# Kernel optimization log

Hardware: AMD Instinct MI355X
Metric: run time of the kernel (lower is better)

Reference implementation:

```python
import jax, jax.numpy as jnp
import numpy as np

B, T, U = 4, 256, 64
D_ENC, D_DEC, V = 512, 512, 1024
IN_F = D_ENC + D_DEC  # 1024


def setup_inputs() -> dict:
    key = jax.random.key(0)
    ks = jax.random.split(key, 10)
    enc = jax.random.normal(ks[0], (B, T, D_ENC), dtype=jnp.float32)
    dec = jax.random.normal(ks[1], (B, U, D_DEC), dtype=jnp.float32)
    # ragged lengths in [len/2, len]; force max to be attained so padded
    # shape equals the torch packed output shape (MaxPad == (T, U)).
    enc_lens = jax.random.randint(ks[2], (B,), T // 2, T + 1, dtype=jnp.int32).at[0].set(T)
    dec_lens = jax.random.randint(ks[3], (B,), U // 2, U + 1, dtype=jnp.int32).at[0].set(U)
    s_e = 1.0 / np.sqrt(D_ENC)
    s_d = 1.0 / np.sqrt(D_DEC)
    s_f = 1.0 / np.sqrt(IN_F)
    W_enc = jax.random.uniform(ks[4], (D_ENC, IN_F), jnp.float32, -s_e, s_e)
    b_enc = jax.random.uniform(ks[5], (IN_F,), jnp.float32, -s_e, s_e)
    W_dec = jax.random.uniform(ks[6], (D_DEC, IN_F), jnp.float32, -s_d, s_d)
    b_dec = jax.random.uniform(ks[7], (IN_F,), jnp.float32, -s_d, s_d)
    W_fc = jax.random.uniform(ks[8], (IN_F, V), jnp.float32, -s_f, s_f)
    b_fc = jax.random.uniform(ks[9], (V,), jnp.float32, -s_f, s_f)
    return dict(enc=enc, dec=dec, W_enc=W_enc, b_enc=b_enc, W_dec=W_dec,
                b_dec=b_dec, W_fc=W_fc, b_fc=b_fc,
                enc_lens=enc_lens, dec_lens=dec_lens)


def reference(enc, dec, W_enc, b_enc, W_dec, b_dec, W_fc, b_fc, enc_lens, dec_lens):
    # per-frame / per-label projections: [B,T,IN_F], [B,U,IN_F]
    pe = jnp.einsum('btd,df->btf', enc, W_enc) + b_enc
    pd = jnp.einsum('bud,df->buf', dec, W_dec) + b_dec
    # broadcast-add joint grid: [B,T,U,IN_F]
    h = pe[:, :, None, :] + pd[:, None, :, :]
    logits = jnp.einsum('btuf,fv->btuv', jnp.tanh(h), W_fc) + b_fc
    logp = jax.nn.log_softmax(logits, axis=-1)
    # zero out cells beyond (enc_len_b, dec_len_b), matching F.pad(value=0.)
    t_ok = jnp.arange(T)[None, :] < enc_lens[:, None]          # [B,T]
    u_ok = jnp.arange(U)[None, :] < dec_lens[:, None]          # [B,U]
    mask = (t_ok[:, :, None] & u_ok[:, None, :])[..., None]    # [B,T,U,1]
    return jnp.where(mask, logp, 0.0)
```

## Files before the change

### kernel.cpp

```cpp
#include <hip/hip_runtime.h>
#include <hip/hip_bf16.h>


#define TT 256
#define UU 64
#define VV 1024
#define FF 1024
#define DK 512

typedef __bf16 bf16x8 __attribute__((ext_vector_type(8)));
typedef float  f32x16 __attribute__((ext_vector_type(16)));
typedef int    i32x4v __attribute__((ext_vector_type(4)));
typedef int    i32x16 __attribute__((ext_vector_type(16)));

__device__ __forceinline__ float fast_tanh(float x) {
  float ax = __builtin_fabsf(x);
  float e  = __expf(-2.0f * ax);
  float r  = (1.0f - e) * __builtin_amdgcn_rcpf(1.0f + e);
  return __builtin_copysignf(r, x);
}

__global__ __launch_bounds__(256)
void prep_w(const float* __restrict__ Wenc, const float* __restrict__ Wdec,
            const float* __restrict__ Wfc,
            __bf16* __restrict__ Pen, __bf16* __restrict__ Pde,
            signed char* __restrict__ Pq, float* __restrict__ sc)
{
  int bi = blockIdx.x;
  int tid = threadIdx.x;
  if (bi < 512) {
    const float* W = (bi < 256) ? Wenc : Wdec;
    __bf16* P = (bi < 256) ? Pen : Pde;
    int base = (bi < 256) ? bi : bi - 256;
    int idx = base * 256 + tid;
    int k8 = idx >> 10, v = idx & 1023;
    bf16x8 o;
#pragma unroll
    for (int j = 0; j < 8; ++j) o[j] = (__bf16)W[(k8 * 8 + j) * 1024 + v];
    *(bf16x8*)(P + (size_t)idx * 8) = o;
    return;
  }
  __shared__ float mx[4][64];
  __shared__ float smax[64];
  int blk = bi - 512;
  int p = tid >> 6;
  int c = tid & 63;
  int v = blk * 64 + c;
  float m = 0.f;
#pragma unroll 8
  for (int k = p * 256; k < p * 256 + 256; ++k)
    m = fmaxf(m, __builtin_fabsf(Wfc[k * 1024 + v]));
  mx[p][c] = m;
  __syncthreads();
  float mm = fmaxf(fmaxf(mx[0][c], mx[1][c]), fmaxf(mx[2][c], mx[3][c]));
  if (p == 0) { smax[c] = mm; sc[v] = (mm > 0.f) ? mm / 127.f : 1.f; }
  __syncthreads();
  float si = (smax[c] > 0.f) ? 127.f / smax[c] : 0.f;
  for (int k16 = p * 16; k16 < p * 16 + 16; ++k16) {
    unsigned int w[4];
#pragma unroll
    for (int g = 0; g < 4; ++g) {
      unsigned int a = 0;
#pragma unroll
      for (int j = 0; j < 4; ++j) {
        float x = Wfc[(k16 * 16 + g * 4 + j) * 1024 + v];
        int q = (int)rintf(x * si);
        q = q > 127 ? 127 : (q < -127 ? -127 : q);
        a |= (unsigned int)(q & 255) << (8 * j);
      }
      w[g] = a;
    }
    *(uint4*)(Pq + ((size_t)k16 * 1024 + v) * 16) = make_uint4(w[0], w[1], w[2], w[3]);
  }
}

__global__ __launch_bounds__(256)
void proj_mfma(const float* __restrict__ enc, const float* __restrict__ dec,
               const __bf16* __restrict__ Pen, const __bf16* __restrict__ Pde,
               const float* __restrict__ be, const float* __restrict__ bd,
               float* __restrict__ pe, float* __restrict__ pd)
{
  constexpr int BK = 128;
  __shared__ __align__(16) char As[2][64 * BK * 2];
  const int tid = threadIdx.x;
  const int lane = tid & 63;
  const int wid  = tid >> 6;
  const int l31  = lane & 31;
  const int lhi  = lane >> 5;

  int bi = blockIdx.x;
  const float* X; const __bf16* PW; const float* bias; float* P; int rt, ct;
  if (bi < 64) { X = enc; PW = Pen; bias = be; P = pe; rt = bi >> 2; ct = bi & 3; }
  else { int bj = bi - 64; X = dec; PW = Pde; bias = bd; P = pd; rt = bj >> 2; ct = bj & 3; }
  const int r0 = rt * 64;

  auto fillA = [&](int buf, int kc) {
#pragma unroll
    for (int i = 0; i < 4; ++i) {
      int tau = i * 256 + tid;
      int r = tau >> 4, g = tau & 15;
      int k = kc * BK + g * 8;
      const float4* x4 = (const float4*)(X + (r0 + r) * DK + k);
      float4 a0 = x4[0], a1 = x4[1];
      float xv[8] = {a0.x, a0.y, a0.z, a0.w, a1.x, a1.y, a1.z, a1.w};
      bf16x8 p;
#pragma unroll
      for (int q = 0; q < 8; ++q) p[q] = (__bf16)xv[q];
      *(bf16x8*)(&As[buf][r * (BK * 2) + ((g * 16) ^ ((r & 7) << 4))]) = p;
    }
  };

  f32x16 acc[2][2];
#pragma unroll
  for (int mi = 0; mi < 2; ++mi)
#pragma unroll
    for (int ni = 0; ni < 2; ++ni)
#pragma unroll
      for (int q = 0; q < 16; ++q) acc[mi][ni][q] = 0.f;

  fillA(0, 0);
  __syncthreads();
  const int colBase = ct * 256 + wid * 64 + l31;
  for (int kc = 0; kc < DK / BK; ++kc) {
    if (kc + 1 < DK / BK) fillA((kc + 1) & 1, kc + 1);
    const char* Ab = As[kc & 1];
#pragma unroll 2
    for (int ks = 0; ks < BK / 16; ++ks) {
      int k8 = (kc * 8 + ks) * 2 + lhi;
      bf16x8 bfr[2];
#pragma unroll
      for (int ni = 0; ni < 2; ++ni)
        bfr[ni] = *(const bf16x8*)(PW + ((size_t)k8 * VV + colBase + ni * 32) * 8);
      bf16x8 afr[2];
#pragma unroll
      for (int mi = 0; mi < 2; ++mi) {
        int ra = mi * 32 + l31;
        int kb = ks * 32 + lhi * 16;
        afr[mi] = *(const bf16x8*)(&Ab[ra * (BK * 2) + (kb ^ ((ra & 7) << 4))]);
      }
#pragma unroll
      for (int mi = 0; mi < 2; ++mi)
#pragma unroll
        for (int ni = 0; ni < 2; ++ni)
          acc[mi][ni] = __builtin_amdgcn_mfma_f32_32x32x16_bf16(afr[mi], bfr[ni], acc[mi][ni], 0, 0, 0);
    }
    __syncthreads();
  }
  float bv[2];
#pragma unroll
  for (int ni = 0; ni < 2; ++ni) bv[ni] = bias[colBase + ni * 32];
#pragma unroll
  for (int mi = 0; mi < 2; ++mi)
#pragma unroll
    for (int j = 0; j < 16; ++j) {
      int row = r0 + mi * 32 + (j & 3) + 8 * (j >> 2) + 4 * lhi;
#pragma unroll
      for (int ni = 0; ni < 2; ++ni)
        P[row * VV + colBase + ni * 32] = acc[mi][ni][j] + bv[ni];
    }
}

__global__ __launch_bounds__(512, 2)
void joint_main(const float* __restrict__ pe, const float* __restrict__ pd,
                const signed char* __restrict__ Pq, const float* __restrict__ sc,
                const float* __restrict__ bfc,
                const int* __restrict__ elens, const int* __restrict__ dlens,
                float* __restrict__ out)
{
  __shared__ __align__(16) unsigned char Bb[4][32768];
  __shared__ __align__(16) unsigned char Ab[2][4096];
  __shared__ float pr[8][64];
  __shared__ float lseS[64];

  const int blk = blockIdx.x;
  const int b = blk >> 8;
  const int t = blk & 255;
  const int tid = threadIdx.x;
  const int elen = elens[b], dlen = dlens[b];
  float* outBase = out + (size_t)blk * (UU * VV);

  if (t >= elen) {
    float4 z = {0.f, 0.f, 0.f, 0.f};
#pragma unroll 4
    for (int i = tid; i < UU * VV / 4; i += 512) ((float4*)outBase)[i] = z;
    return;
  }

  const int lane = tid & 63;
  const int wid  = tid >> 6;
  const int l31  = lane & 31;
  const int lhi  = lane >> 5;
  const int colLane = wid * 128 + l31;

  const float* peRow  = pe + (size_t)blk * FF;
  const float* pdBase = pd + (size_t)b * UU * FF;

  auto stageB = [&](int kc, int buf) {
    const signed char* gp = Pq + (size_t)kc * 32768;
#pragma unroll
    for (int i = 0; i < 4; ++i) {
      int fb = (i >> 1) * 1024 + wid * 128 + (i & 1) * 64;
      __builtin_amdgcn_global_load_lds(
        (const __attribute__((address_space(1))) void*)(gp + ((size_t)fb + lane) * 16),
        (__attribute__((address_space(3))) void*)(&Bb[buf][fb * 16]),
        16, 0, 0);
    }
  };

  float4 R0, R1, R2, R3;
  const int ar = tid >> 3;
  const int ah = tid & 7;
  auto issueA = [&](int s) {
    int k = s * 64 + (ah >> 1) * 16 + (ah & 1) * 8;
    const float4* e4 = (const float4*)(peRow + k);
    const float4* d4 = (const float4*)(pdBase + (size_t)ar * FF + k);
    R0 = e4[0]; R1 = e4[1]; R2 = d4[0]; R3 = d4[1];
  };
  auto commitA = [&](int buf) {
    float hv[8] = {R0.x + R2.x, R0.y + R2.y, R0.z + R2.z, R0.w + R2.w,
                   R1.x + R3.x, R1.y + R3.y, R1.z + R3.z, R1.w + R3.w};
    unsigned int lo = 0, hi = 0;
#pragma unroll
    for (int e = 0; e < 4; ++e) {
      int q = (int)rintf(fast_tanh(hv[e]) * 127.f);
      lo |= (unsigned int)(q & 255) << (8 * e);
    }
#pragma unroll
    for (int e = 0; e < 4; ++e) {
      int q = (int)rintf(fast_tanh(hv[4 + e]) * 127.f);
      hi |= (unsigned int)(q & 255) << (8 * e);
    }
    *(uint2*)(&Ab[buf][(((ah >> 1) << 6) + ar) * 16 + ((ah & 1) << 3)]) =
        make_uint2(lo, hi);
  };

  i32x16 acc[2][4];
#pragma unroll
  for (int mi = 0; mi < 2; ++mi)
#pragma unroll
    for (int ni = 0; ni < 4; ++ni)
#pragma unroll
      for (int q = 0; q < 16; ++q) acc[mi][ni][q] = 0;

  auto mstep = [&](const unsigned char* Bp, const unsigned char* Ap, int kcL) {
    i32x4v bfr[4];
#pragma unroll
    for (int ni = 0; ni < 4; ++ni)
      bfr[ni] = *(const i32x4v*)(Bp + ((size_t)(lhi * 1024 + colLane + (ni << 5)) << 4));
    i32x4v afr[2];
#pragma unroll
    for (int mi = 0; mi < 2; ++mi)
      afr[mi] = *(const i32x4v*)(Ap + ((((kcL << 1) + lhi) << 6) + mi * 32 + l31) * 16);
#pragma unroll
    for (int mi = 0; mi < 2; ++mi)
#pragma unroll
      for (int ni = 0; ni < 4; ++ni)
        acc[mi][ni] = __builtin_amdgcn_mfma_i32_32x32x32_i8(afr[mi], bfr[ni], acc[mi][ni], 0, 0, 0);
  };

  issueA(0);
  commitA(0);
  stageB(0, 0); stageB(1, 1); stageB(2, 2);
  asm volatile("s_waitcnt lgkmcnt(0)" ::: "memory");
  __builtin_amdgcn_sched_barrier(0);
  __builtin_amdgcn_s_barrier();
  __builtin_amdgcn_sched_barrier(0);

#pragma unroll
  for (int kc = 0; kc < 32; ++kc) {
    const int s = kc >> 1;
    if ((kc & 1) == 0 && s + 1 <= 15) {
      issueA(s + 1);
      __builtin_amdgcn_sched_barrier(0);
    }
    if (kc + 3 < 32) {
      stageB(kc + 3, (kc + 3) & 3);
      __builtin_amdgcn_sched_barrier(0);
    }
    if (kc <= 28)      asm volatile("s_waitcnt vmcnt(16)" ::: "memory");
    else if (kc == 29) asm volatile("s_waitcnt vmcnt(12)" ::: "memory");
    else if (kc == 30) asm volatile("s_waitcnt vmcnt(4)"  ::: "memory");
    else               asm volatile("s_waitcnt vmcnt(0)"  ::: "memory");
    __builtin_amdgcn_sched_barrier(0);
    __builtin_amdgcn_s_setprio(1);
    mstep(Bb[kc & 3], Ab[s & 1], kc & 1);
    __builtin_amdgcn_s_setprio(0);
    if ((kc & 1) == 1 && kc < 31) {
      commitA((s + 1) & 1);
      asm volatile("s_waitcnt lgkmcnt(0)" ::: "memory");
      __builtin_amdgcn_sched_barrier(0);
      __builtin_amdgcn_s_barrier();
      __builtin_amdgcn_sched_barrier(0);
    }
  }

  float bias[4], scl[4];
#pragma unroll
  for (int ni = 0; ni < 4; ++ni) {
    bias[ni] = bfc[colLane + ni * 32];
    scl[ni]  = sc[colLane + ni * 32] * (1.f / 127.f);
  }

  float rsum[2][16];
#pragma unroll
  for (int mi = 0; mi < 2; ++mi)
#pragma unroll
    for (int j = 0; j < 16; ++j) {
      float su = 0.f;
#pragma unroll
      for (int ni = 0; ni < 4; ++ni) {
        float v = (float)acc[mi][ni][j] * scl[ni] + bias[ni];
        acc[mi][ni][j] = __float_as_int(v);
        su += __expf(v);
      }
      rsum[mi][j] = su;
    }
#pragma unroll
  for (int st = 1; st < 32; st <<= 1) {
#pragma unroll
    for (int mi = 0; mi < 2; ++mi)
#pragma unroll
      for (int j = 0; j < 16; ++j)
        rsum[mi][j] += __shfl_xor(rsum[mi][j], st, 64);
  }
#pragma unroll
  for (int mi = 0; mi < 2; ++mi)
#pragma unroll
    for (int j = 0; j < 16; ++j)
      if (l31 == j) {
        int row = mi * 32 + (j & 3) + 8 * (j >> 2) + 4 * lhi;
        pr[wid][row] = rsum[mi][j];
      }
  __syncthreads();
  if (tid < 64) {
    float su = 0.f;
#pragma unroll
    for (int w = 0; w < 8; ++w) su += pr[w][tid];
    lseS[tid] = __logf(su);
  }
  __syncthreads();

#pragma unroll
  for (int mi = 0; mi < 2; ++mi)
#pragma unroll
    for (int j = 0; j < 16; ++j) {
      int row = mi * 32 + (j & 3) + 8 * (j >> 2) + 4 * lhi;
      float l = lseS[row];
      bool valid = row < dlen;
#pragma unroll
      for (int ni = 0; ni < 4; ++ni) {
        float v = valid ? (__int_as_float(acc[mi][ni][j]) - l) : 0.0f;
        outBase[(size_t)row * VV + colLane + ni * 32] = v;
      }
    }
}

extern "C" void kernel_launch(void* const* d_in, const int* in_sizes, int n_in,
                              void* d_out, int out_size, void* d_ws, size_t ws_size,
                              hipStream_t stream)
{
  const float* enc  = (const float*)d_in[0];
  const float* dec  = (const float*)d_in[1];
  const float* Wenc = (const float*)d_in[2];
  const float* benc = (const float*)d_in[3];
  const float* Wdec = (const float*)d_in[4];
  const float* bdec = (const float*)d_in[5];
  const float* Wfc  = (const float*)d_in[6];
  const float* bfc  = (const float*)d_in[7];
  const int* elens  = (const int*)d_in[8];
  const int* dlens  = (const int*)d_in[9];
  float* out = (float*)d_out;

  float* pe = (float*)d_ws;
  float* pd = pe + 1024 * 1024;
  __bf16* Pen = (__bf16*)(pd + 256 * 1024);
  __bf16* Pde = Pen + 512 * 1024;
  signed char* Pq = (signed char*)(Pde + 512 * 1024);
  float* sc = (float*)(Pq + 1024 * 1024);

  prep_w<<<528, 256, 0, stream>>>(Wenc, Wdec, Wfc, Pen, Pde, Pq, sc);
  proj_mfma<<<80, 256, 0, stream>>>(enc, dec, Pen, Pde, benc, bdec, pe, pd);
  joint_main<<<1024, 512, 0, stream>>>(pe, pd, Pq, sc, bfc, elens, dlens, out);
}
```

Baseline: 232.4 us.

## Precompute full int8 A tile upfront and stream B fragments via registers

The kernel now builds the entire quantized tanh(pe+pd) A tile (64x1024 int8) in LDS in one prologue pass, followed by a single barrier. The per-stage A issue/commit and the block barriers inside the K loop are gone. B fragments are no longer staged through LDS with global_load_lds. Each wave loads its own B fragments straight from global memory into a 4-deep register ring. This removes LDS traffic for B and most synchronization, but it adds register pressure, loses the overlap between A computation and MMA, and relies on global/L2 latency being hidden by the register prefetch depth.

```diff
diff --git a/kernel.cpp b/kernel.cpp
--- a/kernel.cpp
+++ b/kernel.cpp
@@ -167,8 +167,7 @@
                 const int* __restrict__ elens, const int* __restrict__ dlens,
                 float* __restrict__ out)
 {
-  __shared__ __align__(16) unsigned char Bb[4][32768];
-  __shared__ __align__(16) unsigned char Ab[2][4096];
+  __shared__ __align__(16) unsigned char Ab[65536];
   __shared__ float pr[8][64];
   __shared__ float lseS[64];
 
@@ -195,45 +194,40 @@
   const float* peRow  = pe + (size_t)blk * FF;
   const float* pdBase = pd + (size_t)b * UU * FF;
 
-  auto stageB = [&](int kc, int buf) {
+  {
+    const int row = tid >> 3;
+    const float* pdRow = pdBase + (size_t)row * FF;
+#pragma unroll
+    for (int j = 0; j < 8; ++j) {
+      int k16 = ((tid & 7) << 3) + j;
+      const float4* e4 = (const float4*)(peRow + k16 * 16);
+      const float4* d4 = (const float4*)(pdRow + k16 * 16);
+      unsigned int w[4];
+#pragma unroll
+      for (int g = 0; g < 4; ++g) {
+        float4 e = e4[g], d = d4[g];
+        float h0 = e.x + d.x, h1 = e.y + d.y, h2 = e.z + d.z, h3 = e.w + d.w;
+        unsigned int a = 0;
+        a |= (unsigned int)(((int)rintf(fast_tanh(h0) * 127.f)) & 255);
+        a |= (unsigned int)(((int)rintf(fast_tanh(h1) * 127.f)) & 255) << 8;
+        a |= (unsigned int)(((int)rintf(fast_tanh(h2) * 127.f)) & 255) << 16;
+        a |= (unsigned int)(((int)rintf(fast_tanh(h3) * 127.f)) & 255) << 24;
+        w[g] = a;
+      }
+      *(uint4*)(&Ab[((k16 << 6) + row) << 4]) = make_uint4(w[0], w[1], w[2], w[3]);
+    }
+  }
+  __syncthreads();
+
+  i32x4v bq[4][4];
+  auto loadB = [&](int kc) {
     const signed char* gp = Pq + (size_t)kc * 32768;
 #pragma unroll
-    for (int i = 0; i < 4; ++i) {
-      int fb = (i >> 1) * 1024 + wid * 128 + (i & 1) * 64;
-      __builtin_amdgcn_global_load_lds(
-        (const __attribute__((address_space(1))) void*)(gp + ((size_t)fb + lane) * 16),
-        (__attribute__((address_space(3))) void*)(&Bb[buf][fb * 16]),
-        16, 0, 0);
-    }
+    for (int ni = 0; ni < 4; ++ni)
+      bq[kc & 3][ni] = *(const i32x4v*)(gp +
+          ((size_t)((lhi << 10) + colLane + (ni << 5)) << 4));
   };
 
-  float4 R0, R1, R2, R3;
-  const int ar = tid >> 3;
-  const int ah = tid & 7;
-  auto issueA = [&](int s) {
-    int k = s * 64 + (ah >> 1) * 16 + (ah & 1) * 8;
-    const float4* e4 = (const float4*)(peRow + k);
-    const float4* d4 = (const float4*)(pdBase + (size_t)ar * FF + k);
-    R0 = e4[0]; R1 = e4[1]; R2 = d4[0]; R3 = d4[1];
-  };
-  auto commitA = [&](int buf) {
-    float hv[8] = {R0.x + R2.x, R0.y + R2.y, R0.z + R2.z, R0.w + R2.w,
-                   R1.x + R3.x, R1.y + R3.y, R1.z + R3.z, R1.w + R3.w};
-    unsigned int lo = 0, hi = 0;
-#pragma unroll
-    for (int e = 0; e < 4; ++e) {
-      int q = (int)rintf(fast_tanh(hv[e]) * 127.f);
-      lo |= (unsigned int)(q & 255) << (8 * e);
-    }
-#pragma unroll
-    for (int e = 0; e < 4; ++e) {
-      int q = (int)rintf(fast_tanh(hv[4 + e]) * 127.f);
-      hi |= (unsigned int)(q & 255) << (8 * e);
-    }
-    *(uint2*)(&Ab[buf][(((ah >> 1) << 6) + ar) * 16 + ((ah & 1) << 3)]) =
-        make_uint2(lo, hi);
-  };
-
   i32x16 acc[2][4];
 #pragma unroll
   for (int mi = 0; mi < 2; ++mi)
@@ -242,56 +236,21 @@
 #pragma unroll
       for (int q = 0; q < 16; ++q) acc[mi][ni][q] = 0;
 
-  auto mstep = [&](const unsigned char* Bp, const unsigned char* Ap, int kcL) {
-    i32x4v bfr[4];
-#pragma unroll
-    for (int ni = 0; ni < 4; ++ni)
-      bfr[ni] = *(const i32x4v*)(Bp + ((size_t)(lhi * 1024 + colLane + (ni << 5)) << 4));
+  loadB(0); loadB(1); loadB(2); loadB(3);
+
+#pragma unroll
+  for (int kc = 0; kc < 32; ++kc) {
     i32x4v afr[2];
 #pragma unroll
     for (int mi = 0; mi < 2; ++mi)
-      afr[mi] = *(const i32x4v*)(Ap + ((((kcL << 1) + lhi) << 6) + mi * 32 + l31) * 16);
+      afr[mi] = *(const i32x4v*)(&Ab[((((kc << 1) + lhi) << 6) + mi * 32 + l31) << 4]);
 #pragma unroll
     for (int mi = 0; mi < 2; ++mi)
 #pragma unroll
       for (int ni = 0; ni < 4; ++ni)
-        acc[mi][ni] = __builtin_amdgcn_mfma_i32_32x32x32_i8(afr[mi], bfr[ni], acc[mi][ni], 0, 0, 0);
-  };
-
-  issueA(0);
-  commitA(0);
-  stageB(0, 0); stageB(1, 1); stageB(2, 2);
-  asm volatile("s_waitcnt lgkmcnt(0)" ::: "memory");
-  __builtin_amdgcn_sched_barrier(0);
-  __builtin_amdgcn_s_barrier();
-  __builtin_amdgcn_sched_barrier(0);
-
-#pragma unroll
-  for (int kc = 0; kc < 32; ++kc) {
-    const int s = kc >> 1;
-    if ((kc & 1) == 0 && s + 1 <= 15) {
-      issueA(s + 1);
-      __builtin_amdgcn_sched_barrier(0);
-    }
-    if (kc + 3 < 32) {
-      stageB(kc + 3, (kc + 3) & 3);
-      __builtin_amdgcn_sched_barrier(0);
-    }
-    if (kc <= 28)      asm volatile("s_waitcnt vmcnt(16)" ::: "memory");
-    else if (kc == 29) asm volatile("s_waitcnt vmcnt(12)" ::: "memory");
-    else if (kc == 30) asm volatile("s_waitcnt vmcnt(4)"  ::: "memory");
-    else               asm volatile("s_waitcnt vmcnt(0)"  ::: "memory");
-    __builtin_amdgcn_sched_barrier(0);
-    __builtin_amdgcn_s_setprio(1);
-    mstep(Bb[kc & 3], Ab[s & 1], kc & 1);
-    __builtin_amdgcn_s_setprio(0);
-    if ((kc & 1) == 1 && kc < 31) {
-      commitA((s + 1) & 1);
-      asm volatile("s_waitcnt lgkmcnt(0)" ::: "memory");
-      __builtin_amdgcn_sched_barrier(0);
-      __builtin_amdgcn_s_barrier();
-      __builtin_amdgcn_sched_barrier(0);
-    }
+        acc[mi][ni] = __builtin_amdgcn_mfma_i32_32x32x32_i8(afr[mi], bq[kc & 3][ni],
+                                                            acc[mi][ni], 0, 0, 0);
+    if (kc + 4 < 32) loadB(kc + 4);
   }
 
   float bias[4], scl[4];
```

Result: slower. 240.7 us (+3.6%).
